# Performance work log

Measured on AMD Instinct MI355X. Metric: run time of the kernel, lower is better.

Reference implementation:

```python
import jax, jax.numpy as jnp
import numpy as np
import math

PHI = (1.0 + math.sqrt(5.0)) / 2.0
LN_EPS = 1e-5


def _carrier_phases(n_heads: int) -> np.ndarray:
    """Reproduce DimensionalHeadManager._allocate carrier phases."""
    base = [k * math.pi / 7.0 for k in range(7)]  # rung base phases
    n_rungs = 7
    raw = []
    remaining = n_heads
    for i in range(n_rungs):
        if i < n_rungs - 1:
            c = max(1, round(n_heads / PHI ** (i + 1)))
            c = min(c, remaining - (n_rungs - 1 - i))
            raw.append(c)
            remaining -= c
        else:
            raw.append(max(1, remaining))
    phases = []
    for rung_idx, count in enumerate(raw):
        for j in range(count):
            phases.append(base[rung_idx] + 2.0 * math.pi / max(count, 1) * j)
    return np.asarray(phases[:n_heads], dtype=np.float32)


def setup_inputs() -> dict:
    key = jax.random.key(0)
    ks = jax.random.split(key, 7)
    B, S, D, H = 2, 2048, 1024, 16
    w_scale = 0.02  # realistic init scale for Linear weights
    x = jax.random.normal(ks[0], (B, S, D), dtype=jnp.float32)
    Wq = jax.random.normal(ks[1], (D, D), dtype=jnp.float32) * w_scale
    Wk = jax.random.normal(ks[2], (D, D), dtype=jnp.float32) * w_scale
    Wv = jax.random.normal(ks[3], (D, D), dtype=jnp.float32) * w_scale
    Wo = jax.random.normal(ks[4], (D, D), dtype=jnp.float32) * w_scale
    Wp = jax.random.normal(ks[5], (D,), dtype=jnp.float32) * w_scale  # W_phase (1,D) flattened
    gamma = jnp.ones((D,), dtype=jnp.float32)
    beta = jnp.zeros((D,), dtype=jnp.float32)
    carrier = jnp.asarray(_carrier_phases(H))  # srl.carrier_freq init
    lam = jnp.float32(0.1)  # lambda_resonance init
    return {"x": x, "Wq": Wq, "Wk": Wk, "Wv": Wv, "Wo": Wo, "Wp": Wp,
            "gamma": gamma, "beta": beta, "carrier": carrier, "lam": lam}


def reference(x, Wq, Wk, Wv, Wo, Wp, gamma, beta, carrier, lam):
    B, S, D = x.shape
    H = carrier.shape[0]
    dh = D // H
    scale = 1.0 / math.sqrt(dh)

    residual = x
    # LayerNorm
    mu = jnp.mean(x, axis=-1, keepdims=True)
    var = jnp.mean((x - mu) ** 2, axis=-1, keepdims=True)
    xn = (x - mu) * jax.lax.rsqrt(var + LN_EPS) * gamma + beta

    # Q/K/V projections (torch Linear: y = x @ W.T), split into heads
    q = jnp.einsum('bsd,ed->bse', xn, Wq).reshape(B, S, H, dh)
    k = jnp.einsum('bsd,ed->bse', xn, Wk).reshape(B, S, H, dh)
    v = jnp.einsum('bsd,ed->bse', xn, Wv).reshape(B, S, H, dh)

    # scalar phase per token, per-head carrier resonance gate
    phase = jnp.einsum('bsd,d->bs', xn, Wp)                       # (B,S)
    head_T = jnp.cos((phase[..., None] - carrier) * 0.5) ** 2     # (B,S,H)

    # attention scores + resonance term R_ij = cos^2((phi_i - phi_j)/2)
    scores = jnp.einsum('bihd,bjhd->bhij', q, k) * scale          # (B,H,S,S)
    R = jnp.cos((phase[:, :, None] - phase[:, None, :]) * 0.5) ** 2  # (B,S,S)
    scores = scores + lam * R[:, None, :, :]

    attn = jax.nn.softmax(scores, axis=-1)
    out = jnp.einsum('bhij,bjhd->bihd', attn, v)                  # (B,S,H,dh)
    out = out * head_T[..., None]                                 # per-head resonance gating
    emergent_energy = jnp.sum(jnp.abs(out))
    y = residual + jnp.einsum('bse,de->bsd', out.reshape(B, S, D), Wo)
    return (y, emergent_energy)
```

## Files before the change

### kernel.cpp

```cpp
#include <hip/hip_runtime.h>
#include <hip/hip_bf16.h>

#define S_LEN 2048
#define D_MODEL 1024
#define NH 16
#define DH 64
#define M_TOK 4096
#define DK 80

typedef __attribute__((ext_vector_type(8))) short bf16x8;
typedef __attribute__((ext_vector_type(4))) float f32x4;
typedef __attribute__((ext_vector_type(16))) float f32x16;

#define LOG2E 1.4426950408889634f

__device__ __forceinline__ unsigned short f2bf(float f) {
  unsigned u = __float_as_uint(f);
  u += 0x7FFF + ((u >> 16) & 1);
  return (unsigned short)(u >> 16);
}

__device__ __forceinline__ void gl16(const void* g, void* l) {
  __builtin_amdgcn_global_load_lds(
      (const __attribute__((address_space(1))) unsigned int*)g,
      (__attribute__((address_space(3))) unsigned int*)l, 16, 0, 0);
}

__global__ __launch_bounds__(256) void prep_kernel(
    const float* __restrict__ Wq, const float* __restrict__ Wk,
    const float* __restrict__ Wv, const float* __restrict__ Wo,
    unsigned short* __restrict__ wbf, float* __restrict__ energy) {
  if (blockIdx.x == 0 && threadIdx.x == 0) *energy = 0.f;
  int idx = (blockIdx.x * 256 + threadIdx.x) * 4;
  int wsel = idx >> 20;
  const float* s = (wsel == 0) ? Wq : (wsel == 1) ? Wk : (wsel == 2) ? Wv : Wo;
  int off = idx & 1048575;
  float4 v = *(const float4*)(s + off);
  ushort4 p;
  p.x = f2bf(v.x); p.y = f2bf(v.y); p.z = f2bf(v.z); p.w = f2bf(v.w);
  *(ushort4*)(wbf + idx) = p;
}

__device__ __forceinline__ float block_sum(float v, float* sm) {
#pragma unroll
  for (int o = 32; o > 0; o >>= 1) v += __shfl_xor(v, o, 64);
  int w = threadIdx.x >> 6;
  __syncthreads();
  if ((threadIdx.x & 63) == 0) sm[w] = v;
  __syncthreads();
  return sm[0] + sm[1] + sm[2] + sm[3];
}

__global__ __launch_bounds__(256) void ln_phase_kernel(
    const float* __restrict__ x, const float* __restrict__ Wp,
    const float* __restrict__ gamma, const float* __restrict__ beta,
    unsigned short* __restrict__ xn, float* __restrict__ cosP,
    float* __restrict__ sinP) {
  __shared__ float sm[4];
  int row = blockIdx.x;
  int tid = threadIdx.x;
  float4 v = ((const float4*)(x + (size_t)row * D_MODEL))[tid];
  float mu = block_sum(v.x + v.y + v.z + v.w, sm) * (1.0f / D_MODEL);
  float d0 = v.x - mu, d1 = v.y - mu, d2 = v.z - mu, d3 = v.w - mu;
  float var = block_sum(d0 * d0 + d1 * d1 + d2 * d2 + d3 * d3, sm) * (1.0f / D_MODEL);
  float rinv = rsqrtf(var + 1e-5f);
  float4 g = ((const float4*)gamma)[tid];
  float4 be = ((const float4*)beta)[tid];
  float n0 = d0 * rinv * g.x + be.x;
  float n1 = d1 * rinv * g.y + be.y;
  float n2 = d2 * rinv * g.z + be.z;
  float n3 = d3 * rinv * g.w + be.w;
  ushort4 p;
  p.x = f2bf(n0); p.y = f2bf(n1); p.z = f2bf(n2); p.w = f2bf(n3);
  ((ushort4*)(xn + (size_t)row * D_MODEL))[tid] = p;
  float4 wp = ((const float4*)Wp)[tid];
  float ph = block_sum(n0 * wp.x + n1 * wp.y + n2 * wp.z + n3 * wp.w, sm);
  if (tid == 0) {
    cosP[row] = cosf(ph);
    sinP[row] = sinf(ph);
  }
}

__global__ __launch_bounds__(256) void phase_fill_kernel(
    const float* __restrict__ cosP, const float* __restrict__ sinP,
    unsigned short* __restrict__ kk80) {
  int gid = blockIdx.x * 256 + threadIdx.x;
  int s = gid & (S_LEN - 1);
  int bh = gid >> 11;
  int b = bh >> 4;
  int tok = b * S_LEN + s;
  unsigned int w0 = (unsigned int)f2bf(cosP[tok]) | ((unsigned int)f2bf(sinP[tok]) << 16);
  int4 lo = make_int4((int)w0, 0, 0, 0);
  int4 hi = make_int4(0, 0, 0, 0);
  *(int4*)(kk80 + (size_t)gid * DK + 64) = lo;
  *(int4*)(kk80 + (size_t)gid * DK + 72) = hi;
}

__global__ __launch_bounds__(256) void qkv_gemm_kernel(
    const unsigned short* __restrict__ xn, const unsigned short* __restrict__ wbf,
    unsigned short* __restrict__ q, unsigned short* __restrict__ kk80,
    unsigned short* __restrict__ vT) {
  __shared__ __align__(16) unsigned short As[128 * 64];
  __shared__ __align__(16) unsigned short Bs[128 * 64];
  int z = blockIdx.z;
  const unsigned short* Wm = wbf + (size_t)z * (D_MODEL * D_MODEL);
  const unsigned short* Ap = (z == 2) ? Wm : xn;
  const unsigned short* Bp = (z == 2) ? xn : Wm;
  int m0 = (z == 2) ? blockIdx.x * 128 : blockIdx.y * 128;
  int n0 = (z == 2) ? blockIdx.y * 128 : blockIdx.x * 128;
  int tid = threadIdx.x;
  int wave = tid >> 6, lane = tid & 63, quad = lane >> 4, l15 = lane & 15;
  int wm = (wave & 1) * 64, wn = (wave >> 1) * 64;
  f32x4 acc[4][4];
#pragma unroll
  for (int r = 0; r < 4; ++r)
#pragma unroll
    for (int c = 0; c < 4; ++c) acc[r][c] = (f32x4){0.f, 0.f, 0.f, 0.f};

  for (int k0 = 0; k0 < D_MODEL; k0 += 64) {
    __syncthreads();
#pragma unroll
    for (int t = 0; t < 4; ++t) {
      int c = t * 256 + tid;
      int r = c >> 3, p = c & 7;
      int qc = p ^ (r & 7);
      gl16(&Ap[(size_t)(m0 + r) * D_MODEL + k0 + qc * 8], &As[c * 8]);
      gl16(&Bp[(size_t)(n0 + r) * D_MODEL + k0 + qc * 8], &Bs[c * 8]);
    }
    __syncthreads();
    bf16x8 af[4][2], bfr[4][2];
#pragma unroll
    for (int r = 0; r < 4; ++r) {
      int R = wm + r * 16 + l15;
#pragma unroll
      for (int h = 0; h < 2; ++h)
        af[r][h] = *(const bf16x8*)&As[R * 64 + ((h * 4 + quad) ^ (R & 7)) * 8];
    }
#pragma unroll
    for (int c = 0; c < 4; ++c) {
      int R = wn + c * 16 + l15;
#pragma unroll
      for (int h = 0; h < 2; ++h)
        bfr[c][h] = *(const bf16x8*)&Bs[R * 64 + ((h * 4 + quad) ^ (R & 7)) * 8];
    }
#pragma unroll
    for (int h = 0; h < 2; ++h)
#pragma unroll
      for (int r = 0; r < 4; ++r)
#pragma unroll
        for (int c = 0; c < 4; ++c)
          acc[r][c] = __builtin_amdgcn_mfma_f32_16x16x32_bf16(af[r][h], bfr[c][h], acc[r][c], 0, 0, 0);
  }
#pragma unroll
  for (int r = 0; r < 4; ++r) {
#pragma unroll
    for (int c = 0; c < 4; ++c) {
#pragma unroll
      for (int rr = 0; rr < 4; ++rr) {
        if (z == 2) {
          int e = m0 + wm + r * 16 + quad * 4 + rr;
          int tok = n0 + wn + c * 16 + l15;
          int hh = e >> 6, d = e & 63;
          int bb = tok >> 11, ss = tok & (S_LEN - 1);
          vT[(((size_t)(bb * NH + hh)) * DH + d) * S_LEN + ss] = f2bf(acc[r][c][rr]);
        } else {
          int tok = m0 + wm + r * 16 + quad * 4 + rr;
          int e = n0 + wn + c * 16 + l15;
          int hh = e >> 6, d = e & 63;
          int bb = tok >> 11, ss = tok & (S_LEN - 1);
          if (z == 0) {
            unsigned short val = f2bf(acc[r][c][rr] * (0.125f * LOG2E));
            q[(((size_t)(bb * NH + hh)) * S_LEN + ss) * DH + d] = val;
          } else {
            kk80[(((size_t)(bb * NH + hh)) * S_LEN + ss) * DK + d] = f2bf(acc[r][c][rr]);
          }
        }
      }
    }
  }
}

__global__ __launch_bounds__(256) void attn_kernel(
    const unsigned short* __restrict__ q, const unsigned short* __restrict__ kk80,
    const unsigned short* __restrict__ vT, const float* __restrict__ cosP,
    const float* __restrict__ sinP, const float* __restrict__ carrier,
    const float* __restrict__ lamp, unsigned short* __restrict__ outw,
    float* __restrict__ energy) {
  __shared__ __align__(16) unsigned short Ks[640 * 8];
  __shared__ __align__(16) unsigned short Vs[512 * 8];
  __shared__ __align__(16) unsigned int Ps[4][32 * 34];
  __shared__ float Lr[4][32];
  __shared__ float er[4];
  int qt = blockIdx.x, h = blockIdx.y, b = blockIdx.z;
  int bh = b * NH + h;
  int tid = threadIdx.x, wave = tid >> 6, lane = tid & 63;
  int half = lane >> 5, l31 = lane & 31;

  const unsigned short* kb = kk80 + (size_t)bh * S_LEN * DK;
  const unsigned short* vb = vT + (size_t)bh * DH * S_LEN;
  int qrow = qt * 128 + wave * 32 + l31;

  bf16x8 bQ[5];
  {
    const unsigned short* qp = q + ((size_t)bh * S_LEN + qrow) * DH;
#pragma unroll
    for (int db = 0; db < 4; ++db)
      bQ[db] = *(const bf16x8*)(qp + db * 16 + half * 8);
    bf16x8 z8 = {0, 0, 0, 0, 0, 0, 0, 0};
    if (half == 0) {
      float hl2 = 0.5f * lamp[0] * LOG2E;
      z8[0] = (short)f2bf(hl2 * cosP[b * S_LEN + qrow]);
      z8[1] = (short)f2bf(hl2 * sinP[b * S_LEN + qrow]);
    }
    bQ[4] = z8;
  }

  f32x16 O0 = {}, O1 = {};
  float l_i = 0.f;

  for (int j0 = 0; j0 < S_LEN; j0 += 64) {
    __syncthreads();
#pragma unroll
    for (int t = 0; t < 2; ++t) {
      int cc = t * 256 + tid;
      int r = (cc * 205) >> 11;
      int p = cc - r * 10;
      int g = p + ((r >> 2) & 3);
      if (g >= 10) g -= 10;
      gl16(&kb[(size_t)(j0 + r) * DK + g * 8], (unsigned short*)Ks + cc * 8);
    }
    if (tid < 128) {
      int cc = 512 + tid;
      int r = (cc * 205) >> 11;
      int p = cc - r * 10;
      int g = p + ((r >> 2) & 3);
      if (g >= 10) g -= 10;
      gl16(&kb[(size_t)(j0 + r) * DK + g * 8], (unsigned short*)Ks + cc * 8);
    }
#pragma unroll
    for (int t = 0; t < 2; ++t) {
      int cc = t * 256 + tid;
      int r = cc >> 3, p = cc & 7;
      int g = p ^ (r & 7);
      gl16(&vb[(size_t)r * S_LEN + j0 + g * 8], (unsigned short*)Vs + cc * 8);
    }
    __syncthreads();

    f32x16 Sf[2];
#pragma unroll
    for (int sj = 0; sj < 2; ++sj) {
      Sf[sj] = (f32x16){};
      int r = sj * 32 + l31;
      int rot = (r >> 2) & 3;
#pragma unroll
      for (int db = 0; db < 5; ++db) {
        int p = db * 2 + half - rot;
        if (p < 0) p += 10;
        bf16x8 aK = *(const bf16x8*)((const unsigned short*)Ks + (r * 10 + p) * 8);
        Sf[sj] = __builtin_amdgcn_mfma_f32_32x32x16_bf16(aK, bQ[db], Sf[sj], 0, 0, 0);
      }
    }

#pragma unroll
    for (int sj = 0; sj < 2; ++sj) {
#pragma unroll
      for (int rr = 0; rr < 8; ++rr) {
        float e0 = exp2f(Sf[sj][rr * 2 + 0]);
        float e1 = exp2f(Sf[sj][rr * 2 + 1]);
        l_i += e0 + e1;
        __hip_bfloat162 pk = __float22bfloat162_rn(float2{e0, e1});
        int jd = sj * 16 + (rr >> 1) * 4 + half * 2 + (rr & 1);
        Ps[wave][l31 * 34 + jd] = *(unsigned int*)&pk;
      }
    }

#pragma unroll
    for (int jb = 0; jb < 4; ++jb) {
      const unsigned int* pp = &Ps[wave][l31 * 34 + jb * 8 + half * 4];
      uint2 a0 = *(const uint2*)pp;
      uint2 a1 = *(const uint2*)(pp + 2);
      union { unsigned int u[4]; bf16x8 v; } cvt;
      cvt.u[0] = a0.x; cvt.u[1] = a0.y; cvt.u[2] = a1.x; cvt.u[3] = a1.y;
      {
        int rv = l31;
        int p = (jb * 2 + half) ^ (rv & 7);
        bf16x8 bV = *(const bf16x8*)((const unsigned short*)Vs + (rv * 8 + p) * 8);
        O0 = __builtin_amdgcn_mfma_f32_32x32x16_bf16(cvt.v, bV, O0, 0, 0, 0);
      }
      {
        int rv = 32 + l31;
        int p = (jb * 2 + half) ^ (rv & 7);
        bf16x8 bV = *(const bf16x8*)((const unsigned short*)Vs + (rv * 8 + p) * 8);
        O1 = __builtin_amdgcn_mfma_f32_32x32x16_bf16(cvt.v, bV, O1, 0, 0, 0);
      }
    }
  }

  l_i += __shfl_xor(l_i, 32, 64);
  Lr[wave][l31] = l_i;
  float ch = cosf(carrier[h]), sh = sinf(carrier[h]);
  float esum = 0.f;
#pragma unroll
  for (int reg = 0; reg < 16; ++reg) {
    int ir = (reg & 3) + 8 * (reg >> 2) + 4 * half;
    int srow = qt * 128 + wave * 32 + ir;
    float cp = cosP[b * S_LEN + srow], sp = sinP[b * S_LEN + srow];
    float gate = 0.5f + 0.5f * (cp * ch + sp * sh);
    float gl = gate / Lr[wave][ir];
    size_t tok = (size_t)b * S_LEN + srow;
    float v0 = O0[reg] * gl, v1 = O1[reg] * gl;
    esum += fabsf(v0) + fabsf(v1);
    outw[tok * D_MODEL + h * DH + l31] = f2bf(v0);
    outw[tok * D_MODEL + h * DH + 32 + l31] = f2bf(v1);
  }
#pragma unroll
  for (int off = 32; off > 0; off >>= 1) esum += __shfl_xor(esum, off, 64);
  if (lane == 0) er[wave] = esum;
  __syncthreads();
  if (tid == 0) atomicAdd(energy, er[0] + er[1] + er[2] + er[3]);
}

__global__ __launch_bounds__(256) void out_gemm_kernel(
    const unsigned short* __restrict__ A, const unsigned short* __restrict__ Wo,
    const float* __restrict__ x, float* __restrict__ y) {
  __shared__ __align__(16) unsigned short As[128 * 64];
  __shared__ __align__(16) unsigned short Bs[128 * 64];
  int tid = threadIdx.x;
  int wave = tid >> 6, lane = tid & 63, quad = lane >> 4, l15 = lane & 15;
  int wm = (wave & 1) * 64, wn = (wave >> 1) * 64;
  int m0 = blockIdx.y * 128, n0 = blockIdx.x * 128;
  f32x4 acc[4][4];
#pragma unroll
  for (int r = 0; r < 4; ++r)
#pragma unroll
    for (int c = 0; c < 4; ++c) acc[r][c] = (f32x4){0.f, 0.f, 0.f, 0.f};

  for (int k0 = 0; k0 < D_MODEL; k0 += 64) {
    __syncthreads();
#pragma unroll
    for (int t = 0; t < 4; ++t) {
      int c = t * 256 + tid;
      int r = c >> 3, p = c & 7;
      int qc = p ^ (r & 7);
      gl16(&A[(size_t)(m0 + r) * D_MODEL + k0 + qc * 8], &As[c * 8]);
      gl16(&Wo[(size_t)(n0 + r) * D_MODEL + k0 + qc * 8], &Bs[c * 8]);
    }
    __syncthreads();
    bf16x8 af[4][2], bfr[4][2];
#pragma unroll
    for (int r = 0; r < 4; ++r) {
      int R = wm + r * 16 + l15;
#pragma unroll
      for (int h = 0; h < 2; ++h)
        af[r][h] = *(const bf16x8*)&As[R * 64 + ((h * 4 + quad) ^ (R & 7)) * 8];
    }
#pragma unroll
    for (int c = 0; c < 4; ++c) {
      int R = wn + c * 16 + l15;
#pragma unroll
      for (int h = 0; h < 2; ++h)
        bfr[c][h] = *(const bf16x8*)&Bs[R * 64 + ((h * 4 + quad) ^ (R & 7)) * 8];
    }
#pragma unroll
    for (int h = 0; h < 2; ++h)
#pragma unroll
      for (int r = 0; r < 4; ++r)
#pragma unroll
        for (int c = 0; c < 4; ++c)
          acc[r][c] = __builtin_amdgcn_mfma_f32_16x16x32_bf16(af[r][h], bfr[c][h], acc[r][c], 0, 0, 0);
  }
#pragma unroll
  for (int r = 0; r < 4; ++r) {
#pragma unroll
    for (int c = 0; c < 4; ++c) {
      int dcol = n0 + wn + c * 16 + l15;
#pragma unroll
      for (int rr = 0; rr < 4; ++rr) {
        int tok = m0 + wm + r * 16 + quad * 4 + rr;
        size_t idx = (size_t)tok * D_MODEL + dcol;
        y[idx] = x[idx] + acc[r][c][rr];
      }
    }
  }
}

extern "C" void kernel_launch(void* const* d_in, const int* in_sizes, int n_in,
                              void* d_out, int out_size, void* d_ws, size_t ws_size,
                              hipStream_t stream) {
  const float* x = (const float*)d_in[0];
  const float* Wq = (const float*)d_in[1];
  const float* Wk = (const float*)d_in[2];
  const float* Wv = (const float*)d_in[3];
  const float* Wo = (const float*)d_in[4];
  const float* Wp = (const float*)d_in[5];
  const float* gamma = (const float*)d_in[6];
  const float* beta = (const float*)d_in[7];
  const float* carrier = (const float*)d_in[8];
  const float* lam = (const float*)d_in[9];

  char* ws = (char*)d_ws;
  const size_t MB = 1024 * 1024;
  unsigned short* wbf = (unsigned short*)(ws);
  unsigned short* xn = (unsigned short*)(ws + 8 * MB);
  unsigned short* qq = (unsigned short*)(ws + 16 * MB);
  unsigned short* kk80 = (unsigned short*)(ws + 24 * MB);
  unsigned short* vT = (unsigned short*)(ws + 34 * MB);
  float* cosP = (float*)(ws + 42 * MB);
  float* sinP = (float*)(ws + 42 * MB + 16 * 1024);
  unsigned short* outw = xn;

  float* y = (float*)d_out;
  float* energy = y + (out_size - 1);

  prep_kernel<<<4096, 256, 0, stream>>>(Wq, Wk, Wv, Wo, wbf, energy);
  ln_phase_kernel<<<M_TOK, 256, 0, stream>>>(x, Wp, gamma, beta, xn, cosP, sinP);
  phase_fill_kernel<<<256, 256, 0, stream>>>(cosP, sinP, kk80);
  qkv_gemm_kernel<<<dim3(8, 32, 3), 256, 0, stream>>>(xn, wbf, qq, kk80, vT);
  attn_kernel<<<dim3(16, 16, 2), 256, 0, stream>>>(qq, kk80, vT, cosP, sinP,
                                                   carrier, lam, outw, energy);
  out_gemm_kernel<<<dim3(8, 32), 256, 0, stream>>>(outw, wbf + 3 * D_MODEL * D_MODEL,
                                                   x, y);
}
```

Measured before the change: 242.6 us.

## Retile attention, out GEMM and QKV grid for higher occupancy

The attention kernel moves to 128-thread blocks over 64 query rows, doubling the block count. Its K tile stride drops from 80 to 72 elements, which removes the rotation swizzle and the zero-padding write. The output GEMM uses 128x64 tiles so twice as many blocks launch, and the QKV GEMM becomes a flat 1D grid that treats Q and K as one 2048-wide N dimension, with occupancy hints added. The goal is better CU fill on the many-CU device, at the cost of LDS bank conflicts on the unswizzled 72-stride K tile and less operand reuse per block.

```diff
diff --git a/kernel.cpp b/kernel.cpp
--- a/kernel.cpp
+++ b/kernel.cpp
@@ -90,24 +90,30 @@
   int b = bh >> 4;
   int tok = b * S_LEN + s;
   unsigned int w0 = (unsigned int)f2bf(cosP[tok]) | ((unsigned int)f2bf(sinP[tok]) << 16);
-  int4 lo = make_int4((int)w0, 0, 0, 0);
-  int4 hi = make_int4(0, 0, 0, 0);
-  *(int4*)(kk80 + (size_t)gid * DK + 64) = lo;
-  *(int4*)(kk80 + (size_t)gid * DK + 72) = hi;
-}
-
-__global__ __launch_bounds__(256) void qkv_gemm_kernel(
+  *(int4*)(kk80 + (size_t)gid * DK + 64) = make_int4((int)w0, 0, 0, 0);
+}
+
+__global__ __launch_bounds__(256, 3) void qkv_gemm_kernel(
     const unsigned short* __restrict__ xn, const unsigned short* __restrict__ wbf,
     unsigned short* __restrict__ q, unsigned short* __restrict__ kk80,
     unsigned short* __restrict__ vT) {
   __shared__ __align__(16) unsigned short As[128 * 64];
   __shared__ __align__(16) unsigned short Bs[128 * 64];
-  int z = blockIdx.z;
-  const unsigned short* Wm = wbf + (size_t)z * (D_MODEL * D_MODEL);
-  const unsigned short* Ap = (z == 2) ? Wm : xn;
-  const unsigned short* Bp = (z == 2) ? xn : Wm;
-  int m0 = (z == 2) ? blockIdx.x * 128 : blockIdx.y * 128;
-  int n0 = (z == 2) ? blockIdx.y * 128 : blockIdx.x * 128;
+  int bid = blockIdx.x;
+  bool vmode = bid >= 512;
+  const unsigned short* Ap;
+  const unsigned short* Bp;
+  int m0, n0;
+  if (!vmode) {
+    m0 = (bid >> 4) * 128;
+    n0 = (bid & 15) * 128;
+    Ap = xn; Bp = wbf;
+  } else {
+    int v2 = bid - 512;
+    m0 = (v2 & 7) * 128;
+    n0 = (v2 >> 3) * 128;
+    Ap = wbf + 2 * D_MODEL * D_MODEL; Bp = xn;
+  }
   int tid = threadIdx.x;
   int wave = tid >> 6, lane = tid & 63, quad = lane >> 4, l15 = lane & 15;
   int wm = (wave & 1) * 64, wn = (wave >> 1) * 64;
@@ -123,9 +129,9 @@
     for (int t = 0; t < 4; ++t) {
       int c = t * 256 + tid;
       int r = c >> 3, p = c & 7;
-      int qc = p ^ (r & 7);
-      gl16(&Ap[(size_t)(m0 + r) * D_MODEL + k0 + qc * 8], &As[c * 8]);
-      gl16(&Bp[(size_t)(n0 + r) * D_MODEL + k0 + qc * 8], &Bs[c * 8]);
+      int g = p ^ (r & 7);
+      gl16(&Ap[(size_t)(m0 + r) * D_MODEL + k0 + g * 8], &As[c * 8]);
+      gl16(&Bp[(size_t)(n0 + r) * D_MODEL + k0 + g * 8], &Bs[c * 8]);
     }
     __syncthreads();
     bf16x8 af[4][2], bfr[4][2];
@@ -157,7 +163,7 @@
     for (int c = 0; c < 4; ++c) {
 #pragma unroll
       for (int rr = 0; rr < 4; ++rr) {
-        if (z == 2) {
+        if (vmode) {
           int e = m0 + wm + r * 16 + quad * 4 + rr;
           int tok = n0 + wn + c * 16 + l15;
           int hh = e >> 6, d = e & 63;
@@ -165,12 +171,13 @@
           vT[(((size_t)(bb * NH + hh)) * DH + d) * S_LEN + ss] = f2bf(acc[r][c][rr]);
         } else {
           int tok = m0 + wm + r * 16 + quad * 4 + rr;
-          int e = n0 + wn + c * 16 + l15;
+          int n = n0 + wn + c * 16 + l15;
+          int e = n & 1023;
           int hh = e >> 6, d = e & 63;
           int bb = tok >> 11, ss = tok & (S_LEN - 1);
-          if (z == 0) {
-            unsigned short val = f2bf(acc[r][c][rr] * (0.125f * LOG2E));
-            q[(((size_t)(bb * NH + hh)) * S_LEN + ss) * DH + d] = val;
+          if ((n0 >> 10) == 0) {
+            q[(((size_t)(bb * NH + hh)) * S_LEN + ss) * DH + d] =
+                f2bf(acc[r][c][rr] * (0.125f * LOG2E));
           } else {
             kk80[(((size_t)(bb * NH + hh)) * S_LEN + ss) * DK + d] = f2bf(acc[r][c][rr]);
           }
@@ -180,17 +187,17 @@
   }
 }
 
-__global__ __launch_bounds__(256) void attn_kernel(
+__global__ __launch_bounds__(128, 3) void attn_kernel(
     const unsigned short* __restrict__ q, const unsigned short* __restrict__ kk80,
     const unsigned short* __restrict__ vT, const float* __restrict__ cosP,
     const float* __restrict__ sinP, const float* __restrict__ carrier,
     const float* __restrict__ lamp, unsigned short* __restrict__ outw,
     float* __restrict__ energy) {
-  __shared__ __align__(16) unsigned short Ks[640 * 8];
+  __shared__ __align__(16) unsigned short Ks[64 * 72];
   __shared__ __align__(16) unsigned short Vs[512 * 8];
-  __shared__ __align__(16) unsigned int Ps[4][32 * 34];
-  __shared__ float Lr[4][32];
-  __shared__ float er[4];
+  __shared__ __align__(16) unsigned int Ps[2][32 * 34];
+  __shared__ float Lr[2][32];
+  __shared__ float er[2];
   int qt = blockIdx.x, h = blockIdx.y, b = blockIdx.z;
   int bh = b * NH + h;
   int tid = threadIdx.x, wave = tid >> 6, lane = tid & 63;
@@ -198,7 +205,7 @@
 
   const unsigned short* kb = kk80 + (size_t)bh * S_LEN * DK;
   const unsigned short* vb = vT + (size_t)bh * DH * S_LEN;
-  int qrow = qt * 128 + wave * 32 + l31;
+  int qrow = qt * 64 + wave * 32 + l31;
 
   bf16x8 bQ[5];
   {
@@ -221,25 +228,19 @@
   for (int j0 = 0; j0 < S_LEN; j0 += 64) {
     __syncthreads();
 #pragma unroll
-    for (int t = 0; t < 2; ++t) {
-      int cc = t * 256 + tid;
-      int r = (cc * 205) >> 11;
-      int p = cc - r * 10;
-      int g = p + ((r >> 2) & 3);
-      if (g >= 10) g -= 10;
-      gl16(&kb[(size_t)(j0 + r) * DK + g * 8], (unsigned short*)Ks + cc * 8);
-    }
-    if (tid < 128) {
-      int cc = 512 + tid;
-      int r = (cc * 205) >> 11;
-      int p = cc - r * 10;
-      int g = p + ((r >> 2) & 3);
-      if (g >= 10) g -= 10;
-      gl16(&kb[(size_t)(j0 + r) * DK + g * 8], (unsigned short*)Ks + cc * 8);
-    }
-#pragma unroll
-    for (int t = 0; t < 2; ++t) {
-      int cc = t * 256 + tid;
+    for (int t = 0; t < 4; ++t) {
+      unsigned int cc = t * 128 + tid;
+      unsigned int r = cc / 9u, p = cc - r * 9u;
+      gl16(&kb[(size_t)(j0 + r) * DK + p * 8], (unsigned short*)Ks + cc * 8);
+    }
+    if (tid < 64) {
+      unsigned int cc = 512 + tid;
+      unsigned int r = cc / 9u, p = cc - r * 9u;
+      gl16(&kb[(size_t)(j0 + r) * DK + p * 8], (unsigned short*)Ks + cc * 8);
+    }
+#pragma unroll
+    for (int t = 0; t < 4; ++t) {
+      int cc = t * 128 + tid;
       int r = cc >> 3, p = cc & 7;
       int g = p ^ (r & 7);
       gl16(&vb[(size_t)r * S_LEN + j0 + g * 8], (unsigned short*)Vs + cc * 8);
@@ -251,12 +252,10 @@
     for (int sj = 0; sj < 2; ++sj) {
       Sf[sj] = (f32x16){};
       int r = sj * 32 + l31;
-      int rot = (r >> 2) & 3;
 #pragma unroll
       for (int db = 0; db < 5; ++db) {
-        int p = db * 2 + half - rot;
-        if (p < 0) p += 10;
-        bf16x8 aK = *(const bf16x8*)((const unsigned short*)Ks + (r * 10 + p) * 8);
+        int p = (db < 4) ? (db * 2 + half) : 8;
+        bf16x8 aK = *(const bf16x8*)((const unsigned short*)Ks + (r * 9 + p) * 8);
         Sf[sj] = __builtin_amdgcn_mfma_f32_32x32x16_bf16(aK, bQ[db], Sf[sj], 0, 0, 0);
       }
     }
@@ -303,13 +302,13 @@
 #pragma unroll
   for (int reg = 0; reg < 16; ++reg) {
     int ir = (reg & 3) + 8 * (reg >> 2) + 4 * half;
-    int srow = qt * 128 + wave * 32 + ir;
+    int srow = qt * 64 + wave * 32 + ir;
     float cp = cosP[b * S_LEN + srow], sp = sinP[b * S_LEN + srow];
     float gate = 0.5f + 0.5f * (cp * ch + sp * sh);
     float gl = gate / Lr[wave][ir];
-    size_t tok = (size_t)b * S_LEN + srow;
     float v0 = O0[reg] * gl, v1 = O1[reg] * gl;
     esum += fabsf(v0) + fabsf(v1);
+    size_t tok = (size_t)b * S_LEN + srow;
     outw[tok * D_MODEL + h * DH + l31] = f2bf(v0);
     outw[tok * D_MODEL + h * DH + 32 + l31] = f2bf(v1);
   }
@@ -317,23 +316,23 @@
   for (int off = 32; off > 0; off >>= 1) esum += __shfl_xor(esum, off, 64);
   if (lane == 0) er[wave] = esum;
   __syncthreads();
-  if (tid == 0) atomicAdd(energy, er[0] + er[1] + er[2] + er[3]);
+  if (tid == 0) atomicAdd(energy, er[0] + er[1]);
 }
 
 __global__ __launch_bounds__(256) void out_gemm_kernel(
     const unsigned short* __restrict__ A, const unsigned short* __restrict__ Wo,
     const float* __restrict__ x, float* __restrict__ y) {
   __shared__ __align__(16) unsigned short As[128 * 64];
-  __shared__ __align__(16) unsigned short Bs[128 * 64];
+  __shared__ __align__(16) unsigned short Bs[64 * 64];
   int tid = threadIdx.x;
   int wave = tid >> 6, lane = tid & 63, quad = lane >> 4, l15 = lane & 15;
-  int wm = (wave & 1) * 64, wn = (wave >> 1) * 64;
-  int m0 = blockIdx.y * 128, n0 = blockIdx.x * 128;
-  f32x4 acc[4][4];
+  int wm = (wave & 1) * 64, wn = (wave >> 1) * 32;
+  int m0 = blockIdx.y * 128, n0 = blockIdx.x * 64;
+  f32x4 acc[4][2];
 #pragma unroll
   for (int r = 0; r < 4; ++r)
 #pragma unroll
-    for (int c = 0; c < 4; ++c) acc[r][c] = (f32x4){0.f, 0.f, 0.f, 0.f};
+    for (int c = 0; c < 2; ++c) acc[r][c] = (f32x4){0.f, 0.f, 0.f, 0.f};
 
   for (int k0 = 0; k0 < D_MODEL; k0 += 64) {
     __syncthreads();
@@ -343,10 +342,16 @@
       int r = c >> 3, p = c & 7;
       int qc = p ^ (r & 7);
       gl16(&A[(size_t)(m0 + r) * D_MODEL + k0 + qc * 8], &As[c * 8]);
+    }
+#pragma unroll
+    for (int t = 0; t < 2; ++t) {
+      int c = t * 256 + tid;
+      int r = c >> 3, p = c & 7;
+      int qc = p ^ (r & 7);
       gl16(&Wo[(size_t)(n0 + r) * D_MODEL + k0 + qc * 8], &Bs[c * 8]);
     }
     __syncthreads();
-    bf16x8 af[4][2], bfr[4][2];
+    bf16x8 af[4][2], bfr[2][2];
 #pragma unroll
     for (int r = 0; r < 4; ++r) {
       int R = wm + r * 16 + l15;
@@ -355,7 +360,7 @@
         af[r][h] = *(const bf16x8*)&As[R * 64 + ((h * 4 + quad) ^ (R & 7)) * 8];
     }
 #pragma unroll
-    for (int c = 0; c < 4; ++c) {
+    for (int c = 0; c < 2; ++c) {
       int R = wn + c * 16 + l15;
 #pragma unroll
       for (int h = 0; h < 2; ++h)
@@ -366,13 +371,13 @@
 #pragma unroll
       for (int r = 0; r < 4; ++r)
 #pragma unroll
-        for (int c = 0; c < 4; ++c)
+        for (int c = 0; c < 2; ++c)
           acc[r][c] = __builtin_amdgcn_mfma_f32_16x16x32_bf16(af[r][h], bfr[c][h], acc[r][c], 0, 0, 0);
   }
 #pragma unroll
   for (int r = 0; r < 4; ++r) {
 #pragma unroll
-    for (int c = 0; c < 4; ++c) {
+    for (int c = 0; c < 2; ++c) {
       int dcol = n0 + wn + c * 16 + l15;
 #pragma unroll
       for (int rr = 0; rr < 4; ++rr) {
@@ -415,9 +420,9 @@
   prep_kernel<<<4096, 256, 0, stream>>>(Wq, Wk, Wv, Wo, wbf, energy);
   ln_phase_kernel<<<M_TOK, 256, 0, stream>>>(x, Wp, gamma, beta, xn, cosP, sinP);
   phase_fill_kernel<<<256, 256, 0, stream>>>(cosP, sinP, kk80);
-  qkv_gemm_kernel<<<dim3(8, 32, 3), 256, 0, stream>>>(xn, wbf, qq, kk80, vT);
-  attn_kernel<<<dim3(16, 16, 2), 256, 0, stream>>>(qq, kk80, vT, cosP, sinP,
+  qkv_gemm_kernel<<<768, 256, 0, stream>>>(xn, wbf, qq, kk80, vT);
+  attn_kernel<<<dim3(32, 16, 2), 128, 0, stream>>>(qq, kk80, vT, cosP, sinP,
                                                    carrier, lam, outw, energy);
-  out_gemm_kernel<<<dim3(8, 32), 256, 0, stream>>>(outw, wbf + 3 * D_MODEL * D_MODEL,
-                                                   x, y);
-}
+  out_gemm_kernel<<<dim3(16, 32), 256, 0, stream>>>(outw, wbf + 3 * D_MODEL * D_MODEL,
+                                                    x, y);
+}
```

Measured after the change: 228.5 us. -5.8%, faster.
